# Kernel tuning notes

Hardware: AMD Instinct MI355X
Metric: run time of the kernel (lower is better)

Reference implementation:

```python
import jax, jax.numpy as jnp
import numpy as np

N, E, B = 50000, 800000, 512
IN, H, OUT = 128, 64, 32
BN_EPS = 1e-5


def setup_inputs() -> dict:
    key = jax.random.key(0)
    ks = jax.random.split(key, 32)
    inp = {}
    inp["x"] = jax.random.normal(ks[0], (N, IN), dtype=jnp.float32)
    inp["edge_index"] = jax.random.randint(ks[1], (2, E), 0, N, dtype=jnp.int64)
    inp["batch"] = jnp.sort(jax.random.randint(ks[2], (N,), 0, B, dtype=jnp.int64))
    inp["batch_size"] = B
    # GINConv MLP params: Linear(cin,H) -> BN(H) -> ReLU -> Linear(H,H)
    cins = [IN, H, H]
    ki = 3
    for i, cin in enumerate(cins):
        inp[f"c{i}_W1"] = jax.random.normal(ks[ki], (cin, H), dtype=jnp.float32) / np.sqrt(cin); ki += 1
        inp[f"c{i}_b1"] = jnp.zeros((H,), jnp.float32)
        inp[f"c{i}_g1"] = jnp.ones((H,), jnp.float32)
        inp[f"c{i}_bt1"] = jnp.zeros((H,), jnp.float32)
        inp[f"c{i}_W2"] = jax.random.normal(ks[ki], (H, H), dtype=jnp.float32) / np.sqrt(H); ki += 1
        inp[f"c{i}_b2"] = jnp.zeros((H,), jnp.float32)
    # final MLP (norm=None): Linear(H,H) -> ReLU -> [dropout, eval: identity] -> Linear(H,OUT)
    inp["f_W1"] = jax.random.normal(ks[ki], (H, H), dtype=jnp.float32) / np.sqrt(H); ki += 1
    inp["f_b1"] = jnp.zeros((H,), jnp.float32)
    inp["f_W2"] = jax.random.normal(ks[ki], (H, OUT), dtype=jnp.float32) / np.sqrt(H)
    inp["f_b2"] = jnp.zeros((OUT,), jnp.float32)
    return inp


def _bn(h, g, bt):
    # BatchNorm1d, training-mode statistics (biased variance), eps=1e-5
    mean = h.mean(axis=0)
    var = ((h - mean) ** 2).mean(axis=0)
    return g * (h - mean) * jax.lax.rsqrt(var + BN_EPS) + bt


def _gin_conv(x, src, dst, W1, b1, g1, bt1, W2, b2):
    # sum-aggregate neighbor features: agg[i] = sum_{(j->i)} x[j]
    agg = jax.ops.segment_sum(x[src], dst, num_segments=N)  # [N,H_in]
    h = x + agg  # (1+eps)*x + agg, eps=0
    h = jax.nn.relu(_bn(h @ W1 + b1, g1, bt1))
    return h @ W2 + b2


def reference(x, edge_index, batch, batch_size,
              c0_W1, c0_b1, c0_g1, c0_bt1, c0_W2, c0_b2,
              c1_W1, c1_b1, c1_g1, c1_bt1, c1_W2, c1_b2,
              c2_W1, c2_b1, c2_g1, c2_bt1, c2_W2, c2_b2,
              f_W1, f_b1, f_W2, f_b2):
    src, dst = edge_index[0], edge_index[1]
    convs = [(c0_W1, c0_b1, c0_g1, c0_bt1, c0_W2, c0_b2),
             (c1_W1, c1_b1, c1_g1, c1_bt1, c1_W2, c1_b2),
             (c2_W1, c2_b1, c2_g1, c2_bt1, c2_W2, c2_b2)]
    for p in convs:
        x = jax.nn.relu(_gin_conv(x, src, dst, *p))
    # global_add_pool over graph ids
    pooled = jax.ops.segment_sum(x, batch, num_segments=batch_size)  # [B,H]
    h = jax.nn.relu(pooled @ f_W1 + f_b1)  # dropout=0.5 skipped (eval mode)
    return h @ f_W2 + f_b2  # [B,OUT]
```

## Files before the change

### kernel.cpp

```cpp
#include <hip/hip_runtime.h>
#include <hip/hip_fp16.h>

#define NN 50000
#define EE 800000
#define BB 512
#define DIN 128
#define HH 64
#define DOUT 32
#define BN_EPS 1e-5f
#define SCAN_BLOCKS 196
#define GATHER_BLOCKS 2048
#define PADMAX (16 * NN + EE + 64)

template <int CIN>
__global__ __launch_bounds__(256) void proj_kernel(const float* __restrict__ X,
                                                   const float* __restrict__ W,
                                                   __half2* __restrict__ Qh)
{
    __shared__ float sW[CIN * 64];
    __shared__ float sX[16 * CIN];
    const int tid = threadIdx.x;
    const int row0 = blockIdx.x * 16;

    for (int i = tid; i < CIN * 16; i += 256)
        ((float4*)sW)[i] = ((const float4*)W)[i];
    const float* Xb = X + (size_t)row0 * CIN;
    for (int i = tid; i < 16 * CIN / 4; i += 256)
        ((float4*)sX)[i] = ((const float4*)Xb)[i];
    __syncthreads();

    const int col2 = tid & 31;
    const int rg   = tid >> 5;
    float2 acc0 = {0.f, 0.f};
    float2 acc1 = {0.f, 0.f};
    const float* x0p = &sX[(rg * 2 + 0) * CIN];
    const float* x1p = &sX[(rg * 2 + 1) * CIN];
#pragma unroll 4
    for (int k = 0; k < CIN; ++k) {
        const float2 w = *(const float2*)&sW[k * 64 + col2 * 2];
        const float x0 = x0p[k];
        const float x1 = x1p[k];
        acc0.x = fmaf(x0, w.x, acc0.x);
        acc0.y = fmaf(x0, w.y, acc0.y);
        acc1.x = fmaf(x1, w.x, acc1.x);
        acc1.y = fmaf(x1, w.y, acc1.y);
    }
    const int r0 = row0 + rg * 2;
    Qh[(size_t)(r0 + 0) * 32 + col2] = __floats2half2_rn(acc0.x, acc0.y);
    Qh[(size_t)(r0 + 1) * 32 + col2] = __floats2half2_rn(acc1.x, acc1.y);
}

__global__ __launch_bounds__(256) void fill_kernel(unsigned int* __restrict__ dstw,
                                                   int* __restrict__ deg)
{
    const int i = blockIdx.x * 256 + threadIdx.x;
    if (i < PADMAX / 2) dstw[i] = 0xC350C350u;
    if (i < NN) deg[i] = 0;
}

__global__ __launch_bounds__(256) void hist_rank_kernel(const int* __restrict__ dst,
                                                        int* __restrict__ deg,
                                                        unsigned short* __restrict__ rank)
{
    const int e = blockIdx.x * 256 + threadIdx.x;
    rank[e] = (unsigned short)atomicAdd(&deg[dst[e]], 1);
}

__global__ __launch_bounds__(256) void scanA_kernel(const int* __restrict__ deg,
                                                    int* __restrict__ poffs,
                                                    int* __restrict__ blockSums)
{
    __shared__ int s[256];
    const int t = threadIdx.x;
    const int i = blockIdx.x * 256 + t;
    int v = 0;
    if (i < NN) {
        const int d = deg[i];
        v = (d <= 16) ? 16 : ((d + 15) & ~15);
    }
    s[t] = v;
    __syncthreads();
    for (int off = 1; off < 256; off <<= 1) {
        const int a = (t >= off) ? s[t - off] : 0;
        __syncthreads();
        s[t] += a;
        __syncthreads();
    }
    if (i < NN) poffs[i] = s[t] - v;
    if (t == 255) blockSums[blockIdx.x] = s[255];
}

__global__ __launch_bounds__(256) void scanB_kernel(const int* __restrict__ blockSums,
                                                    int* __restrict__ blockOff,
                                                    int* __restrict__ poffs)
{
    __shared__ int s[256];
    const int t = threadIdx.x;
    const int v = (t < SCAN_BLOCKS) ? blockSums[t] : 0;
    s[t] = v;
    __syncthreads();
    for (int off = 1; off < 256; off <<= 1) {
        const int a = (t >= off) ? s[t - off] : 0;
        __syncthreads();
        s[t] += a;
        __syncthreads();
    }
    if (t < SCAN_BLOCKS) blockOff[t] = s[t] - v;
    if (t == SCAN_BLOCKS - 1) poffs[NN] = s[t];
}

__global__ __launch_bounds__(256) void scanC_kernel(int* __restrict__ poffs,
                                                    const int* __restrict__ blockOff,
                                                    float* __restrict__ statsbuf,
                                                    float* __restrict__ pooled,
                                                    unsigned int* __restrict__ qzero)
{
    const int i = blockIdx.x * 256 + threadIdx.x;
    if (i < NN) poffs[i] += blockOff[blockIdx.x];
    if (i < 384) statsbuf[i] = 0.f;
    if (i < BB * 64) pooled[i] = 0.f;
    if (blockIdx.x == 1 && threadIdx.x < 32) qzero[threadIdx.x] = 0u;
}

__global__ __launch_bounds__(256) void scatter_kernel(const int* __restrict__ src,
                                                      const int* __restrict__ dst,
                                                      const unsigned short* __restrict__ rank,
                                                      const int* __restrict__ poffs,
                                                      unsigned short* __restrict__ srcPadded)
{
    const int e = blockIdx.x * 256 + threadIdx.x;
    const int pos = poffs[dst[e]] + (int)rank[e];
    srcPadded[pos] = (unsigned short)src[e];
}

__global__ __launch_bounds__(256) void gather_kernel(const __half2* __restrict__ Qh,
                                                     const int* __restrict__ poffs,
                                                     const unsigned short* __restrict__ srcPadded,
                                                     const float* __restrict__ b1,
                                                     float* __restrict__ Z,
                                                     float* __restrict__ sums,
                                                     float* __restrict__ sumsq)
{
    const int tid   = threadIdx.x;
    const int lane  = tid & 63;
    const int wid   = tid >> 6;
    const int c     = lane & 31;
    const int grp   = lane >> 5;
    const int shamt = grp << 4;
    const uint* Qd  = (const uint*)Qh;
    const float2 bb = ((const float2*)b1)[c];

    float2 sa = {0.f, 0.f};
    float2 ta = {0.f, 0.f};
    const int step = GATHER_BLOCKS * 4;

    int node = blockIdx.x * 4 + wid;
    int p0 = poffs[node];
    int p1 = poffs[node + 1];
    uint4 ia = *(const uint4*)(srcPadded + p0);
    uint4 ib = *(const uint4*)(srcPadded + p0 + 8);
    bool two = (p1 - p0) > 16;
    uint4 ia2 = {0, 0, 0, 0}, ib2 = {0, 0, 0, 0};
    if (two) {
        ia2 = *(const uint4*)(srcPadded + p0 + 16);
        ib2 = *(const uint4*)(srcPadded + p0 + 24);
    }
    uint sr = Qd[(size_t)node * 32 + c];

    while (true) {
        uint r[16];
#pragma unroll
        for (int k = 0; k < 4; ++k) {
            r[k]     = Qd[(size_t)(((&ia.x)[k] >> shamt) & 0xffffu) * 32 + c];
            r[4 + k] = Qd[(size_t)(((&ib.x)[k] >> shamt) & 0xffffu) * 32 + c];
        }
        if (two) {
#pragma unroll
            for (int k = 0; k < 4; ++k) {
                r[8 + k]  = Qd[(size_t)(((&ia2.x)[k] >> shamt) & 0xffffu) * 32 + c];
                r[12 + k] = Qd[(size_t)(((&ib2.x)[k] >> shamt) & 0xffffu) * 32 + c];
            }
        }

        const int nnode = node + step;
        const bool more = nnode < NN;
        int np0 = 0, np1 = 0;
        uint4 nia = {0, 0, 0, 0}, nib = {0, 0, 0, 0};
        uint4 nia2 = {0, 0, 0, 0}, nib2 = {0, 0, 0, 0};
        uint nsr = 0;
        bool ntwo = false;
        if (more) {
            np0 = poffs[nnode];
            np1 = poffs[nnode + 1];
            nia = *(const uint4*)(srcPadded + np0);
            nib = *(const uint4*)(srcPadded + np0 + 8);
            ntwo = (np1 - np0) > 16;
            if (ntwo) {
                nia2 = *(const uint4*)(srcPadded + np0 + 16);
                nib2 = *(const uint4*)(srcPadded + np0 + 24);
            }
            nsr = Qd[(size_t)nnode * 32 + c];
        }

        float2 acc = {0.f, 0.f};
#pragma unroll
        for (int k = 0; k < 8; ++k) {
            const float2 p = __half22float2(*(const __half2*)&r[k]);
            acc.x += p.x;
            acc.y += p.y;
        }
        if (two) {
#pragma unroll
            for (int k = 8; k < 16; ++k) {
                const float2 p = __half22float2(*(const __half2*)&r[k]);
                acc.x += p.x;
                acc.y += p.y;
            }
        }
        for (int j = p0 + 32; j < p1; j += 16) {
            const uint4 ja = *(const uint4*)(srcPadded + j);
            const uint4 jb = *(const uint4*)(srcPadded + j + 8);
            uint rr[8];
#pragma unroll
            for (int k = 0; k < 4; ++k) {
                rr[k]     = Qd[(size_t)(((&ja.x)[k] >> shamt) & 0xffffu) * 32 + c];
                rr[4 + k] = Qd[(size_t)(((&jb.x)[k] >> shamt) & 0xffffu) * 32 + c];
            }
#pragma unroll
            for (int k = 0; k < 8; ++k) {
                const float2 p = __half22float2(*(const __half2*)&rr[k]);
                acc.x += p.x;
                acc.y += p.y;
            }
        }

        acc.x += __shfl_xor(acc.x, 32);
        acc.y += __shfl_xor(acc.y, 32);

        if (grp == 0) {
            const float2 p = __half22float2(*(const __half2*)&sr);
            acc.x += p.x + bb.x;
            acc.y += p.y + bb.y;
            ((float2*)Z)[(size_t)node * 32 + c] = acc;
            sa.x += acc.x; sa.y += acc.y;
            ta.x += acc.x * acc.x; ta.y += acc.y * acc.y;
        }

        if (!more) break;
        node = nnode; p0 = np0; p1 = np1;
        ia = nia; ib = nib; two = ntwo;
        if (two) { ia2 = nia2; ib2 = nib2; }
        sr = nsr;
    }

    __shared__ float red[4][32][4];
    if (grp == 0) {
        float* rp = red[wid][c];
        rp[0] = sa.x; rp[1] = sa.y; rp[2] = ta.x; rp[3] = ta.y;
    }
    __syncthreads();
    if (tid < 128) {
        const int c2 = tid >> 2;
        const int k  = tid & 3;
        const float v = red[0][c2][k] + red[1][c2][k] + red[2][c2][k] + red[3][c2][k];
        float* dstp;
        if (k == 0)      dstp = &sums[2 * c2 + 0];
        else if (k == 1) dstp = &sums[2 * c2 + 1];
        else if (k == 2) dstp = &sumsq[2 * c2 + 0];
        else             dstp = &sumsq[2 * c2 + 1];
        atomicAdd(dstp, v);
    }
}

__global__ __launch_bounds__(256) void gemm2proj_kernel(const float* __restrict__ Z,
                                                        const float* __restrict__ sums,
                                                        const float* __restrict__ sumsq,
                                                        const float* __restrict__ g1,
                                                        const float* __restrict__ bt1,
                                                        const float* __restrict__ W2,
                                                        const float* __restrict__ b2,
                                                        const float* __restrict__ W1n,
                                                        __half2* __restrict__ QhOut)
{
    __shared__ float sW2[64 * 64];
    __shared__ float sW1[64 * 64];
    __shared__ float sH[16 * 64];
    __shared__ float sA[16 * 64];
    __shared__ float sScale[64];
    __shared__ float sShift[64];
    const int tid = threadIdx.x;
    const int row0 = blockIdx.x * 16;

    if (tid < 64) {
        const float inv_n = 1.0f / (float)NN;
        const float mean = sums[tid] * inv_n;
        const float var = fmaxf(sumsq[tid] * inv_n - mean * mean, 0.f);
        const float sc = g1[tid] * rsqrtf(var + BN_EPS);
        sScale[tid] = sc;
        sShift[tid] = bt1[tid] - mean * sc;
    }
    for (int i = tid; i < 1024; i += 256) {
        ((float4*)sW2)[i] = ((const float4*)W2)[i];
        ((float4*)sW1)[i] = ((const float4*)W1n)[i];
    }
    __syncthreads();

    const float4* Zb = (const float4*)(Z + (size_t)row0 * 64);
    {
        const int i = tid;
        const float4 z = Zb[i];
        const int c4 = i & 15;
        const float4 sc = ((const float4*)sScale)[c4];
        const float4 sh = ((const float4*)sShift)[c4];
        float4 h;
        h.x = fmaxf(fmaf(z.x, sc.x, sh.x), 0.f);
        h.y = fmaxf(fmaf(z.y, sc.y, sh.y), 0.f);
        h.z = fmaxf(fmaf(z.z, sc.z, sh.z), 0.f);
        h.w = fmaxf(fmaf(z.w, sc.w, sh.w), 0.f);
        ((float4*)sH)[i] = h;
    }
    __syncthreads();

    {
        const int col = tid & 63;
        const int r0  = tid >> 6;
        const float bc = b2[col];
        float acc[4] = {bc, bc, bc, bc};
        for (int k = 0; k < 64; k += 4) {
            const float w0 = sW2[(k + 0) * 64 + col];
            const float w1 = sW2[(k + 1) * 64 + col];
            const float w2 = sW2[(k + 2) * 64 + col];
            const float w3 = sW2[(k + 3) * 64 + col];
#pragma unroll
            for (int rr = 0; rr < 4; ++rr) {
                const float4 hv = *(const float4*)&sH[(r0 + rr * 4) * 64 + k];
                acc[rr] = fmaf(hv.x, w0, acc[rr]);
                acc[rr] = fmaf(hv.y, w1, acc[rr]);
                acc[rr] = fmaf(hv.z, w2, acc[rr]);
                acc[rr] = fmaf(hv.w, w3, acc[rr]);
            }
        }
#pragma unroll
        for (int rr = 0; rr < 4; ++rr)
            sA[(r0 + rr * 4) * 64 + col] = fmaxf(acc[rr], 0.f);
    }
    __syncthreads();

    {
        const int col2 = tid & 31;
        const int rg   = tid >> 5;
        float2 acc0 = {0.f, 0.f};
        float2 acc1 = {0.f, 0.f};
        const float* a0p = &sA[(rg * 2 + 0) * 64];
        const float* a1p = &sA[(rg * 2 + 1) * 64];
#pragma unroll 4
        for (int k = 0; k < 64; ++k) {
            const float2 w = *(const float2*)&sW1[k * 64 + col2 * 2];
            const float a0 = a0p[k];
            const float a1 = a1p[k];
            acc0.x = fmaf(a0, w.x, acc0.x);
            acc0.y = fmaf(a0, w.y, acc0.y);
            acc1.x = fmaf(a1, w.x, acc1.x);
            acc1.y = fmaf(a1, w.y, acc1.y);
        }
        const int r0 = row0 + rg * 2;
        QhOut[(size_t)(r0 + 0) * 32 + col2] = __floats2half2_rn(acc0.x, acc0.y);
        QhOut[(size_t)(r0 + 1) * 32 + col2] = __floats2half2_rn(acc1.x, acc1.y);
    }
}

__global__ __launch_bounds__(256) void gemm2pool_kernel(const float* __restrict__ Z,
                                                        const float* __restrict__ sums,
                                                        const float* __restrict__ sumsq,
                                                        const float* __restrict__ g1,
                                                        const float* __restrict__ bt1,
                                                        const float* __restrict__ W2,
                                                        const float* __restrict__ b2,
                                                        const int* __restrict__ batch,
                                                        float* __restrict__ out)
{
    __shared__ float sW[64 * 64];
    __shared__ float sH[16 * 64];
    __shared__ float sScale[64];
    __shared__ float sShift[64];
    const int tid = threadIdx.x;
    const int row0 = blockIdx.x * 16;

    if (tid < 64) {
        const float inv_n = 1.0f / (float)NN;
        const float mean = sums[tid] * inv_n;
        const float var = fmaxf(sumsq[tid] * inv_n - mean * mean, 0.f);
        const float sc = g1[tid] * rsqrtf(var + BN_EPS);
        sScale[tid] = sc;
        sShift[tid] = bt1[tid] - mean * sc;
    }
    for (int i = tid; i < 1024; i += 256)
        ((float4*)sW)[i] = ((const float4*)W2)[i];
    __syncthreads();

    const float4* Zb = (const float4*)(Z + (size_t)row0 * 64);
    {
        const int i = tid;
        const float4 z = Zb[i];
        const int c4 = i & 15;
        const float4 sc = ((const float4*)sScale)[c4];
        const float4 sh = ((const float4*)sShift)[c4];
        float4 h;
        h.x = fmaxf(fmaf(z.x, sc.x, sh.x), 0.f);
        h.y = fmaxf(fmaf(z.y, sc.y, sh.y), 0.f);
        h.z = fmaxf(fmaf(z.z, sc.z, sh.z), 0.f);
        h.w = fmaxf(fmaf(z.w, sc.w, sh.w), 0.f);
        ((float4*)sH)[i] = h;
    }
    __syncthreads();

    const int col = tid & 63;
    const int r0  = tid >> 6;
    const float bc = b2[col];
    float acc[4] = {bc, bc, bc, bc};
    for (int k = 0; k < 64; k += 4) {
        const float w0 = sW[(k + 0) * 64 + col];
        const float w1 = sW[(k + 1) * 64 + col];
        const float w2 = sW[(k + 2) * 64 + col];
        const float w3 = sW[(k + 3) * 64 + col];
#pragma unroll
        for (int rr = 0; rr < 4; ++rr) {
            const float4 hv = *(const float4*)&sH[(r0 + rr * 4) * 64 + k];
            acc[rr] = fmaf(hv.x, w0, acc[rr]);
            acc[rr] = fmaf(hv.y, w1, acc[rr]);
            acc[rr] = fmaf(hv.z, w2, acc[rr]);
            acc[rr] = fmaf(hv.w, w3, acc[rr]);
        }
    }
#pragma unroll
    for (int rr = 0; rr < 4; ++rr) {
        const int row = row0 + r0 + rr * 4;
        const float v = fmaxf(acc[rr], 0.f);
        atomicAdd(&out[(size_t)batch[row] * 64 + col], v);
    }
}

__global__ __launch_bounds__(256) void final_mlp(const float* __restrict__ P,
                                                 const float* __restrict__ W1,
                                                 const float* __restrict__ b1,
                                                 const float* __restrict__ W2,
                                                 const float* __restrict__ b2,
                                                 float* __restrict__ out)
{
    __shared__ float sW1[64 * 64];
    __shared__ float sW2[64 * 32];
    __shared__ float sH[4 * 64];
    const int tid = threadIdx.x;
    const int row0 = blockIdx.x * 4;

    for (int i = tid; i < 1024; i += 256) ((float4*)sW1)[i] = ((const float4*)W1)[i];
    for (int i = tid; i < 512; i += 256) ((float4*)sW2)[i] = ((const float4*)W2)[i];
    __syncthreads();

    const int col = tid & 63;
    const int r = tid >> 6;
    float acc = b1[col];
    const float* prow = P + (size_t)(row0 + r) * 64;
    for (int k = 0; k < 64; ++k) acc = fmaf(prow[k], sW1[k * 64 + col], acc);
    sH[r * 64 + col] = fmaxf(acc, 0.f);
    __syncthreads();

    if (tid < 128) {
        const int c = tid & 31;
        const int r2 = tid >> 5;
        float a2 = b2[c];
        for (int k = 0; k < 64; ++k) a2 = fmaf(sH[r2 * 64 + k], sW2[k * 32 + c], a2);
        out[(size_t)(row0 + r2) * 32 + c] = a2;
    }
}

extern "C" void kernel_launch(void* const* d_in, const int* in_sizes, int n_in,
                              void* d_out, int out_size, void* d_ws, size_t ws_size,
                              hipStream_t stream)
{
    const float* x   = (const float*)d_in[0];
    const int* ei    = (const int*)d_in[1];
    const int* batch = (const int*)d_in[2];
    const float* cW1[3] = {(const float*)d_in[4],  (const float*)d_in[10], (const float*)d_in[16]};
    const float* cb1[3] = {(const float*)d_in[5],  (const float*)d_in[11], (const float*)d_in[17]};
    const float* cg1[3] = {(const float*)d_in[6],  (const float*)d_in[12], (const float*)d_in[18]};
    const float* cbt[3] = {(const float*)d_in[7],  (const float*)d_in[13], (const float*)d_in[19]};
    const float* cW2[3] = {(const float*)d_in[8],  (const float*)d_in[14], (const float*)d_in[20]};
    const float* cb2[3] = {(const float*)d_in[9],  (const float*)d_in[15], (const float*)d_in[21]};
    const float* fW1 = (const float*)d_in[22];
    const float* fb1 = (const float*)d_in[23];
    const float* fW2 = (const float*)d_in[24];
    const float* fb2 = (const float*)d_in[25];
    float* out = (float*)d_out;

    float* bufX     = (float*)d_ws;
    __half2* Qh     = (__half2*)(bufX + (size_t)NN * 64);
    float* pooled   = (float*)(Qh + (size_t)(NN + 1) * 32);
    float* statsbuf = pooled + (size_t)BB * 64;
    int* deg        = (int*)(statsbuf + 384);
    int* poffs      = deg + NN;
    int* blockSums  = poffs + (NN + 1);
    int* blockOff   = blockSums + 256;
    uintptr_t pa = ((uintptr_t)(blockOff + 256) + 15) & ~(uintptr_t)15;
    unsigned short* srcPadded = (unsigned short*)pa;
    unsigned short* rank      = srcPadded + PADMAX;

    const int* esrc = ei;
    const int* edst = ei + EE;

    const int gemm_blocks = NN / 16;
    const int edge_blocks = EE / 256;

    fill_kernel<<<(PADMAX / 2 + 255) / 256, 256, 0, stream>>>((unsigned int*)srcPadded, deg);
    hist_rank_kernel<<<edge_blocks, 256, 0, stream>>>(edst, deg, rank);
    scanA_kernel<<<SCAN_BLOCKS, 256, 0, stream>>>(deg, poffs, blockSums);
    scanB_kernel<<<1, 256, 0, stream>>>(blockSums, blockOff, poffs);
    scanC_kernel<<<SCAN_BLOCKS, 256, 0, stream>>>(poffs, blockOff, statsbuf, pooled,
                                                  (unsigned int*)(Qh + (size_t)NN * 32));
    scatter_kernel<<<edge_blocks, 256, 0, stream>>>(esrc, edst, rank, poffs, srcPadded);

    proj_kernel<DIN><<<gemm_blocks, 256, 0, stream>>>(x, cW1[0], Qh);

    for (int layer = 0; layer < 3; ++layer) {
        float* sums  = statsbuf + layer * 128;
        float* sumsq = sums + 64;

        gather_kernel<<<GATHER_BLOCKS, 256, 0, stream>>>(Qh, poffs, srcPadded, cb1[layer],
                                                         bufX, sums, sumsq);

        if (layer < 2) {
            gemm2proj_kernel<<<gemm_blocks, 256, 0, stream>>>(bufX, sums, sumsq, cg1[layer],
                                                              cbt[layer], cW2[layer], cb2[layer],
                                                              cW1[layer + 1], Qh);
        } else {
            gemm2pool_kernel<<<gemm_blocks, 256, 0, stream>>>(bufX, sums, sumsq, cg1[layer],
                                                              cbt[layer], cW2[layer], cb2[layer],
                                                              batch, pooled);
        }
    }

    final_mlp<<<BB / 4, 256, 0, stream>>>(pooled, fW1, fb1, fW2, fb2, out);
}
```

Baseline: 350.9 us.

## Split projected features into two column planes and gather each plane separately

Stores the fp16 projected features as two 16-column planes instead of one 32-column row, and runs the gather kernel twice per layer, once per plane, so each pass's random-access working set is half the size and more of it fits in cache. Each wave now processes 4 edges in parallel with 16 lanes each and reduces across lanes with an extra shuffle. Index, offset and output accesses use nontemporal loads and stores so they do not evict the feature planes. The cost is an extra kernel launch per layer and reading the CSR index arrays twice.

```diff
diff --git a/kernel.cpp b/kernel.cpp
--- a/kernel.cpp
+++ b/kernel.cpp
@@ -12,10 +12,13 @@
 #define GATHER_BLOCKS 2048
 #define PADMAX (16 * NN + EE + 64)
 
+typedef unsigned int u32x4 __attribute__((ext_vector_type(4)));
+
 template <int CIN>
 __global__ __launch_bounds__(256) void proj_kernel(const float* __restrict__ X,
                                                    const float* __restrict__ W,
-                                                   __half2* __restrict__ Qh)
+                                                   __half2* __restrict__ QhA,
+                                                   __half2* __restrict__ QhB)
 {
     __shared__ float sW[CIN * 64];
     __shared__ float sX[16 * CIN];
@@ -46,8 +49,10 @@
         acc1.y = fmaf(x1, w.y, acc1.y);
     }
     const int r0 = row0 + rg * 2;
-    Qh[(size_t)(r0 + 0) * 32 + col2] = __floats2half2_rn(acc0.x, acc0.y);
-    Qh[(size_t)(r0 + 1) * 32 + col2] = __floats2half2_rn(acc1.x, acc1.y);
+    __half2* plane = (col2 < 16) ? QhA : QhB;
+    const int pc = col2 & 15;
+    plane[(size_t)(r0 + 0) * 16 + pc] = __floats2half2_rn(acc0.x, acc0.y);
+    plane[(size_t)(r0 + 1) * 16 + pc] = __floats2half2_rn(acc1.x, acc1.y);
 }
 
 __global__ __launch_bounds__(256) void fill_kernel(unsigned int* __restrict__ dstw,
@@ -113,13 +118,15 @@
                                                     const int* __restrict__ blockOff,
                                                     float* __restrict__ statsbuf,
                                                     float* __restrict__ pooled,
-                                                    unsigned int* __restrict__ qzero)
+                                                    unsigned int* __restrict__ qzA,
+                                                    unsigned int* __restrict__ qzB)
 {
     const int i = blockIdx.x * 256 + threadIdx.x;
     if (i < NN) poffs[i] += blockOff[blockIdx.x];
     if (i < 384) statsbuf[i] = 0.f;
     if (i < BB * 64) pooled[i] = 0.f;
-    if (blockIdx.x == 1 && threadIdx.x < 32) qzero[threadIdx.x] = 0u;
+    if (blockIdx.x == 1 && threadIdx.x < 16) qzA[threadIdx.x] = 0u;
+    if (blockIdx.x == 2 && threadIdx.x < 16) qzB[threadIdx.x] = 0u;
 }
 
 __global__ __launch_bounds__(256) void scatter_kernel(const int* __restrict__ src,
@@ -133,7 +140,8 @@
     srcPadded[pos] = (unsigned short)src[e];
 }
 
-__global__ __launch_bounds__(256) void gather_kernel(const __half2* __restrict__ Qh,
+template <int PLANE>
+__global__ __launch_bounds__(256) void gather_kernel(const __half2* __restrict__ Qp,
                                                      const int* __restrict__ poffs,
                                                      const unsigned short* __restrict__ srcPadded,
                                                      const float* __restrict__ b1,
@@ -141,99 +149,113 @@
                                                      float* __restrict__ sums,
                                                      float* __restrict__ sumsq)
 {
-    const int tid   = threadIdx.x;
-    const int lane  = tid & 63;
-    const int wid   = tid >> 6;
-    const int c     = lane & 31;
-    const int grp   = lane >> 5;
-    const int shamt = grp << 4;
-    const uint* Qd  = (const uint*)Qh;
-    const float2 bb = ((const float2*)b1)[c];
+    const int tid  = threadIdx.x;
+    const int lane = tid & 63;
+    const int wid  = tid >> 6;
+    const int c    = lane & 15;
+    const int grp  = lane >> 4;
+    const int wsel = grp >> 1;
+    const int sh   = (grp & 1) << 4;
+    const uint* Qd = (const uint*)Qp;
+    const float2 bb = ((const float2*)b1)[PLANE * 16 + c];
 
     float2 sa = {0.f, 0.f};
     float2 ta = {0.f, 0.f};
     const int step = GATHER_BLOCKS * 4;
 
     int node = blockIdx.x * 4 + wid;
-    int p0 = poffs[node];
-    int p1 = poffs[node + 1];
-    uint4 ia = *(const uint4*)(srcPadded + p0);
-    uint4 ib = *(const uint4*)(srcPadded + p0 + 8);
+    int p0 = __builtin_nontemporal_load(poffs + node);
+    int p1 = __builtin_nontemporal_load(poffs + node + 1);
+    u32x4 ia = __builtin_nontemporal_load((const u32x4*)(srcPadded + p0));
+    u32x4 ib = __builtin_nontemporal_load((const u32x4*)(srcPadded + p0 + 8));
     bool two = (p1 - p0) > 16;
-    uint4 ia2 = {0, 0, 0, 0}, ib2 = {0, 0, 0, 0};
+    u32x4 ia2 = {0, 0, 0, 0}, ib2 = {0, 0, 0, 0};
     if (two) {
-        ia2 = *(const uint4*)(srcPadded + p0 + 16);
-        ib2 = *(const uint4*)(srcPadded + p0 + 24);
-    }
-    uint sr = Qd[(size_t)node * 32 + c];
+        ia2 = __builtin_nontemporal_load((const u32x4*)(srcPadded + p0 + 16));
+        ib2 = __builtin_nontemporal_load((const u32x4*)(srcPadded + p0 + 24));
+    }
+    uint sr = Qd[(size_t)node * 16 + c];
 
     while (true) {
-        uint r[16];
-#pragma unroll
-        for (int k = 0; k < 4; ++k) {
-            r[k]     = Qd[(size_t)(((&ia.x)[k] >> shamt) & 0xffffu) * 32 + c];
-            r[4 + k] = Qd[(size_t)(((&ib.x)[k] >> shamt) & 0xffffu) * 32 + c];
+        uint r[8];
+        {
+            const uint i0 = (ia[wsel] >> sh) & 0xffffu;
+            const uint i1 = (ia[2 + wsel] >> sh) & 0xffffu;
+            const uint i2 = (ib[wsel] >> sh) & 0xffffu;
+            const uint i3 = (ib[2 + wsel] >> sh) & 0xffffu;
+            r[0] = Qd[(size_t)i0 * 16 + c];
+            r[1] = Qd[(size_t)i1 * 16 + c];
+            r[2] = Qd[(size_t)i2 * 16 + c];
+            r[3] = Qd[(size_t)i3 * 16 + c];
         }
         if (two) {
-#pragma unroll
-            for (int k = 0; k < 4; ++k) {
-                r[8 + k]  = Qd[(size_t)(((&ia2.x)[k] >> shamt) & 0xffffu) * 32 + c];
-                r[12 + k] = Qd[(size_t)(((&ib2.x)[k] >> shamt) & 0xffffu) * 32 + c];
-            }
+            const uint i4 = (ia2[wsel] >> sh) & 0xffffu;
+            const uint i5 = (ia2[2 + wsel] >> sh) & 0xffffu;
+            const uint i6 = (ib2[wsel] >> sh) & 0xffffu;
+            const uint i7 = (ib2[2 + wsel] >> sh) & 0xffffu;
+            r[4] = Qd[(size_t)i4 * 16 + c];
+            r[5] = Qd[(size_t)i5 * 16 + c];
+            r[6] = Qd[(size_t)i6 * 16 + c];
+            r[7] = Qd[(size_t)i7 * 16 + c];
         }
 
         const int nnode = node + step;
         const bool more = nnode < NN;
         int np0 = 0, np1 = 0;
-        uint4 nia = {0, 0, 0, 0}, nib = {0, 0, 0, 0};
-        uint4 nia2 = {0, 0, 0, 0}, nib2 = {0, 0, 0, 0};
+        u32x4 nia = {0, 0, 0, 0}, nib = {0, 0, 0, 0};
+        u32x4 nia2 = {0, 0, 0, 0}, nib2 = {0, 0, 0, 0};
         uint nsr = 0;
         bool ntwo = false;
         if (more) {
-            np0 = poffs[nnode];
-            np1 = poffs[nnode + 1];
-            nia = *(const uint4*)(srcPadded + np0);
-            nib = *(const uint4*)(srcPadded + np0 + 8);
+            np0 = __builtin_nontemporal_load(poffs + nnode);
+            np1 = __builtin_nontemporal_load(poffs + nnode + 1);
+            nia = __builtin_nontemporal_load((const u32x4*)(srcPadded + np0));
+            nib = __builtin_nontemporal_load((const u32x4*)(srcPadded + np0 + 8));
             ntwo = (np1 - np0) > 16;
             if (ntwo) {
-                nia2 = *(const uint4*)(srcPadded + np0 + 16);
-                nib2 = *(const uint4*)(srcPadded + np0 + 24);
+                nia2 = __builtin_nontemporal_load((const u32x4*)(srcPadded + np0 + 16));
+                nib2 = __builtin_nontemporal_load((const u32x4*)(srcPadded + np0 + 24));
             }
-            nsr = Qd[(size_t)nnode * 32 + c];
+            nsr = Qd[(size_t)nnode * 16 + c];
         }
 
         float2 acc = {0.f, 0.f};
 #pragma unroll
-        for (int k = 0; k < 8; ++k) {
+        for (int k = 0; k < 4; ++k) {
             const float2 p = __half22float2(*(const __half2*)&r[k]);
             acc.x += p.x;
             acc.y += p.y;
         }
         if (two) {
 #pragma unroll
-            for (int k = 8; k < 16; ++k) {
+            for (int k = 4; k < 8; ++k) {
                 const float2 p = __half22float2(*(const __half2*)&r[k]);
                 acc.x += p.x;
                 acc.y += p.y;
             }
         }
         for (int j = p0 + 32; j < p1; j += 16) {
-            const uint4 ja = *(const uint4*)(srcPadded + j);
-            const uint4 jb = *(const uint4*)(srcPadded + j + 8);
-            uint rr[8];
+            const u32x4 ja = __builtin_nontemporal_load((const u32x4*)(srcPadded + j));
+            const u32x4 jb = __builtin_nontemporal_load((const u32x4*)(srcPadded + j + 8));
+            const uint i0 = (ja[wsel] >> sh) & 0xffffu;
+            const uint i1 = (ja[2 + wsel] >> sh) & 0xffffu;
+            const uint i2 = (jb[wsel] >> sh) & 0xffffu;
+            const uint i3 = (jb[2 + wsel] >> sh) & 0xffffu;
+            uint rr[4];
+            rr[0] = Qd[(size_t)i0 * 16 + c];
+            rr[1] = Qd[(size_t)i1 * 16 + c];
+            rr[2] = Qd[(size_t)i2 * 16 + c];
+            rr[3] = Qd[(size_t)i3 * 16 + c];
 #pragma unroll
             for (int k = 0; k < 4; ++k) {
-                rr[k]     = Qd[(size_t)(((&ja.x)[k] >> shamt) & 0xffffu) * 32 + c];
-                rr[4 + k] = Qd[(size_t)(((&jb.x)[k] >> shamt) & 0xffffu) * 32 + c];
-            }
-#pragma unroll
-            for (int k = 0; k < 8; ++k) {
                 const float2 p = __half22float2(*(const __half2*)&rr[k]);
                 acc.x += p.x;
                 acc.y += p.y;
             }
         }
 
+        acc.x += __shfl_xor(acc.x, 16);
+        acc.y += __shfl_xor(acc.y, 16);
         acc.x += __shfl_xor(acc.x, 32);
         acc.y += __shfl_xor(acc.y, 32);
 
@@ -241,7 +263,8 @@
             const float2 p = __half22float2(*(const __half2*)&sr);
             acc.x += p.x + bb.x;
             acc.y += p.y + bb.y;
-            ((float2*)Z)[(size_t)node * 32 + c] = acc;
+            double* zp = (double*)&((float2*)Z)[(size_t)node * 32 + PLANE * 16 + c];
+            __builtin_nontemporal_store(*(double*)&acc, zp);
             sa.x += acc.x; sa.y += acc.y;
             ta.x += acc.x * acc.x; ta.y += acc.y * acc.y;
         }
@@ -253,21 +276,21 @@
         sr = nsr;
     }
 
-    __shared__ float red[4][32][4];
+    __shared__ float red[4][16][4];
     if (grp == 0) {
         float* rp = red[wid][c];
         rp[0] = sa.x; rp[1] = sa.y; rp[2] = ta.x; rp[3] = ta.y;
     }
     __syncthreads();
-    if (tid < 128) {
+    if (tid < 64) {
         const int c2 = tid >> 2;
         const int k  = tid & 3;
         const float v = red[0][c2][k] + red[1][c2][k] + red[2][c2][k] + red[3][c2][k];
         float* dstp;
-        if (k == 0)      dstp = &sums[2 * c2 + 0];
-        else if (k == 1) dstp = &sums[2 * c2 + 1];
-        else if (k == 2) dstp = &sumsq[2 * c2 + 0];
-        else             dstp = &sumsq[2 * c2 + 1];
+        if (k == 0)      dstp = &sums[PLANE * 32 + 2 * c2 + 0];
+        else if (k == 1) dstp = &sums[PLANE * 32 + 2 * c2 + 1];
+        else if (k == 2) dstp = &sumsq[PLANE * 32 + 2 * c2 + 0];
+        else             dstp = &sumsq[PLANE * 32 + 2 * c2 + 1];
         atomicAdd(dstp, v);
     }
 }
@@ -280,7 +303,8 @@
                                                         const float* __restrict__ W2,
                                                         const float* __restrict__ b2,
                                                         const float* __restrict__ W1n,
-                                                        __half2* __restrict__ QhOut)
+                                                        __half2* __restrict__ QhA,
+                                                        __half2* __restrict__ QhB)
 {
     __shared__ float sW2[64 * 64];
     __shared__ float sW1[64 * 64];
@@ -364,8 +388,10 @@
             acc1.y = fmaf(a1, w.y, acc1.y);
         }
         const int r0 = row0 + rg * 2;
-        QhOut[(size_t)(r0 + 0) * 32 + col2] = __floats2half2_rn(acc0.x, acc0.y);
-        QhOut[(size_t)(r0 + 1) * 32 + col2] = __floats2half2_rn(acc1.x, acc1.y);
+        __half2* plane = (col2 < 16) ? QhA : QhB;
+        const int pc = col2 & 15;
+        plane[(size_t)(r0 + 0) * 16 + pc] = __floats2half2_rn(acc0.x, acc0.y);
+        plane[(size_t)(r0 + 1) * 16 + pc] = __floats2half2_rn(acc1.x, acc1.y);
     }
 }
 
@@ -494,8 +520,9 @@
     float* out = (float*)d_out;
 
     float* bufX     = (float*)d_ws;
-    __half2* Qh     = (__half2*)(bufX + (size_t)NN * 64);
-    float* pooled   = (float*)(Qh + (size_t)(NN + 1) * 32);
+    __half2* QhA    = (__half2*)(bufX + (size_t)NN * 64);
+    __half2* QhB    = QhA + (size_t)(NN + 1) * 16;
+    float* pooled   = (float*)(QhB + (size_t)(NN + 1) * 16);
     float* statsbuf = pooled + (size_t)BB * 64;
     int* deg        = (int*)(statsbuf + 384);
     int* poffs      = deg + NN;
@@ -516,22 +543,25 @@
     scanA_kernel<<<SCAN_BLOCKS, 256, 0, stream>>>(deg, poffs, blockSums);
     scanB_kernel<<<1, 256, 0, stream>>>(blockSums, blockOff, poffs);
     scanC_kernel<<<SCAN_BLOCKS, 256, 0, stream>>>(poffs, blockOff, statsbuf, pooled,
-                                                  (unsigned int*)(Qh + (size_t)NN * 32));
+                                                  (unsigned int*)(QhA + (size_t)NN * 16),
+                                                  (unsigned int*)(QhB + (size_t)NN * 16));
     scatter_kernel<<<edge_blocks, 256, 0, stream>>>(esrc, edst, rank, poffs, srcPadded);
 
-    proj_kernel<DIN><<<gemm_blocks, 256, 0, stream>>>(x, cW1[0], Qh);
+    proj_kernel<DIN><<<gemm_blocks, 256, 0, stream>>>(x, cW1[0], QhA, QhB);
 
     for (int layer = 0; layer < 3; ++layer) {
         float* sums  = statsbuf + layer * 128;
         float* sumsq = sums + 64;
 
-        gather_kernel<<<GATHER_BLOCKS, 256, 0, stream>>>(Qh, poffs, srcPadded, cb1[layer],
-                                                         bufX, sums, sumsq);
+        gather_kernel<0><<<GATHER_BLOCKS, 256, 0, stream>>>(QhA, poffs, srcPadded, cb1[layer],
+                                                            bufX, sums, sumsq);
+        gather_kernel<1><<<GATHER_BLOCKS, 256, 0, stream>>>(QhB, poffs, srcPadded, cb1[layer],
+                                                            bufX, sums, sumsq);
 
         if (layer < 2) {
             gemm2proj_kernel<<<gemm_blocks, 256, 0, stream>>>(bufX, sums, sumsq, cg1[layer],
                                                               cbt[layer], cW2[layer], cb2[layer],
-                                                              cW1[layer + 1], Qh);
+                                                              cW1[layer + 1], QhA, QhB);
         } else {
             gemm2pool_kernel<<<gemm_blocks, 256, 0, stream>>>(bufX, sums, sumsq, cg1[layer],
                                                               cbt[layer], cW2[layer], cb2[layer],
```

New measurement: 418.3 us. +19.2%, slower.

## Restructure gather lane mapping to 8-byte row loads and add nontemporal hints

Applied to the files above, without the earlier changes.

The gather kernel now assigns 16 lanes per row, each fetching 8 bytes (four half features), with four edge groups per wave. Previously it used 32 lanes fetching 4 bytes each, with two edge groups packed via 16-bit index shifts. Each lane now loads its own 16-bit neighbour index directly. The partial sums are reduced with two xor shuffles instead of one. Nontemporal load/store builtins are added across the streaming kernels (fill, histogram, scatter, gather, Z reads) to reduce cache pollution, though the index loads are now many small scalar loads instead of uint4 vectors.

```diff
diff --git a/kernel.cpp b/kernel.cpp
--- a/kernel.cpp
+++ b/kernel.cpp
@@ -11,6 +11,9 @@
 #define SCAN_BLOCKS 196
 #define GATHER_BLOCKS 2048
 #define PADMAX (16 * NN + EE + 64)
+
+typedef float f32x4 __attribute__((ext_vector_type(4)));
+typedef unsigned int u32x4 __attribute__((ext_vector_type(4)));
 
 template <int CIN>
 __global__ __launch_bounds__(256) void proj_kernel(const float* __restrict__ X,
@@ -54,7 +57,7 @@
                                                    int* __restrict__ deg)
 {
     const int i = blockIdx.x * 256 + threadIdx.x;
-    if (i < PADMAX / 2) dstw[i] = 0xC350C350u;
+    if (i < PADMAX / 2) __builtin_nontemporal_store(0xC350C350u, dstw + i);
     if (i < NN) deg[i] = 0;
 }
 
@@ -63,7 +66,9 @@
                                                         unsigned short* __restrict__ rank)
 {
     const int e = blockIdx.x * 256 + threadIdx.x;
-    rank[e] = (unsigned short)atomicAdd(&deg[dst[e]], 1);
+    const int d = __builtin_nontemporal_load(dst + e);
+    const unsigned short r = (unsigned short)atomicAdd(&deg[d], 1);
+    __builtin_nontemporal_store(r, rank + e);
 }
 
 __global__ __launch_bounds__(256) void scanA_kernel(const int* __restrict__ deg,
@@ -129,8 +134,11 @@
                                                       unsigned short* __restrict__ srcPadded)
 {
     const int e = blockIdx.x * 256 + threadIdx.x;
-    const int pos = poffs[dst[e]] + (int)rank[e];
-    srcPadded[pos] = (unsigned short)src[e];
+    const int d = __builtin_nontemporal_load(dst + e);
+    const int s = __builtin_nontemporal_load(src + e);
+    const int r = (int)__builtin_nontemporal_load(rank + e);
+    const int pos = poffs[d] + r;
+    srcPadded[pos] = (unsigned short)s;
 }
 
 __global__ __launch_bounds__(256) void gather_kernel(const __half2* __restrict__ Qh,
@@ -141,133 +149,129 @@
                                                      float* __restrict__ sums,
                                                      float* __restrict__ sumsq)
 {
-    const int tid   = threadIdx.x;
-    const int lane  = tid & 63;
-    const int wid   = tid >> 6;
-    const int c     = lane & 31;
-    const int grp   = lane >> 5;
-    const int shamt = grp << 4;
-    const uint* Qd  = (const uint*)Qh;
-    const float2 bb = ((const float2*)b1)[c];
-
-    float2 sa = {0.f, 0.f};
-    float2 ta = {0.f, 0.f};
+    const int tid  = threadIdx.x;
+    const int lane = tid & 63;
+    const int wid  = tid >> 6;
+    const int colq = lane & 15;
+    const int grp  = lane >> 4;
+    const uint2* Qr = (const uint2*)Qh;
+    const float4 bb = ((const float4*)b1)[colq];
+
+    float sa0 = 0.f, sa1 = 0.f, sa2 = 0.f, sa3 = 0.f;
+    float ta0 = 0.f, ta1 = 0.f, ta2 = 0.f, ta3 = 0.f;
     const int step = GATHER_BLOCKS * 4;
 
     int node = blockIdx.x * 4 + wid;
-    int p0 = poffs[node];
-    int p1 = poffs[node + 1];
-    uint4 ia = *(const uint4*)(srcPadded + p0);
-    uint4 ib = *(const uint4*)(srcPadded + p0 + 8);
+    int p0 = __builtin_nontemporal_load(poffs + node);
+    int p1 = __builtin_nontemporal_load(poffs + node + 1);
+    int i0 = __builtin_nontemporal_load(srcPadded + p0 + grp);
+    int i1 = __builtin_nontemporal_load(srcPadded + p0 + 4 + grp);
+    int i2 = __builtin_nontemporal_load(srcPadded + p0 + 8 + grp);
+    int i3 = __builtin_nontemporal_load(srcPadded + p0 + 12 + grp);
     bool two = (p1 - p0) > 16;
-    uint4 ia2 = {0, 0, 0, 0}, ib2 = {0, 0, 0, 0};
+    int i4 = NN, i5 = NN, i6 = NN, i7 = NN;
     if (two) {
-        ia2 = *(const uint4*)(srcPadded + p0 + 16);
-        ib2 = *(const uint4*)(srcPadded + p0 + 24);
-    }
-    uint sr = Qd[(size_t)node * 32 + c];
+        i4 = __builtin_nontemporal_load(srcPadded + p0 + 16 + grp);
+        i5 = __builtin_nontemporal_load(srcPadded + p0 + 20 + grp);
+        i6 = __builtin_nontemporal_load(srcPadded + p0 + 24 + grp);
+        i7 = __builtin_nontemporal_load(srcPadded + p0 + 28 + grp);
+    }
+    uint2 sr = Qr[(size_t)node * 16 + colq];
+
+#define ACC4(r)                                                            \
+    do {                                                                   \
+        const float2 pA_ = __half22float2(*(const __half2*)&(r).x);        \
+        const float2 pB_ = __half22float2(*(const __half2*)&(r).y);        \
+        a0 += pA_.x; a1 += pA_.y; a2 += pB_.x; a3 += pB_.y;                \
+    } while (0)
 
     while (true) {
-        uint r[16];
-#pragma unroll
-        for (int k = 0; k < 4; ++k) {
-            r[k]     = Qd[(size_t)(((&ia.x)[k] >> shamt) & 0xffffu) * 32 + c];
-            r[4 + k] = Qd[(size_t)(((&ib.x)[k] >> shamt) & 0xffffu) * 32 + c];
-        }
+        const uint2 r0 = Qr[(size_t)i0 * 16 + colq];
+        const uint2 r1 = Qr[(size_t)i1 * 16 + colq];
+        const uint2 r2 = Qr[(size_t)i2 * 16 + colq];
+        const uint2 r3 = Qr[(size_t)i3 * 16 + colq];
+        uint2 r4, r5, r6, r7;
         if (two) {
-#pragma unroll
-            for (int k = 0; k < 4; ++k) {
-                r[8 + k]  = Qd[(size_t)(((&ia2.x)[k] >> shamt) & 0xffffu) * 32 + c];
-                r[12 + k] = Qd[(size_t)(((&ib2.x)[k] >> shamt) & 0xffffu) * 32 + c];
-            }
+            r4 = Qr[(size_t)i4 * 16 + colq];
+            r5 = Qr[(size_t)i5 * 16 + colq];
+            r6 = Qr[(size_t)i6 * 16 + colq];
+            r7 = Qr[(size_t)i7 * 16 + colq];
         }
 
         const int nnode = node + step;
         const bool more = nnode < NN;
         int np0 = 0, np1 = 0;
-        uint4 nia = {0, 0, 0, 0}, nib = {0, 0, 0, 0};
-        uint4 nia2 = {0, 0, 0, 0}, nib2 = {0, 0, 0, 0};
-        uint nsr = 0;
+        int ni0 = NN, ni1 = NN, ni2 = NN, ni3 = NN, ni4 = NN, ni5 = NN, ni6 = NN, ni7 = NN;
+        uint2 nsr = {0, 0};
         bool ntwo = false;
         if (more) {
-            np0 = poffs[nnode];
-            np1 = poffs[nnode + 1];
-            nia = *(const uint4*)(srcPadded + np0);
-            nib = *(const uint4*)(srcPadded + np0 + 8);
+            np0 = __builtin_nontemporal_load(poffs + nnode);
+            np1 = __builtin_nontemporal_load(poffs + nnode + 1);
+            ni0 = __builtin_nontemporal_load(srcPadded + np0 + grp);
+            ni1 = __builtin_nontemporal_load(srcPadded + np0 + 4 + grp);
+            ni2 = __builtin_nontemporal_load(srcPadded + np0 + 8 + grp);
+            ni3 = __builtin_nontemporal_load(srcPadded + np0 + 12 + grp);
             ntwo = (np1 - np0) > 16;
             if (ntwo) {
-                nia2 = *(const uint4*)(srcPadded + np0 + 16);
-                nib2 = *(const uint4*)(srcPadded + np0 + 24);
+                ni4 = __builtin_nontemporal_load(srcPadded + np0 + 16 + grp);
+                ni5 = __builtin_nontemporal_load(srcPadded + np0 + 20 + grp);
+                ni6 = __builtin_nontemporal_load(srcPadded + np0 + 24 + grp);
+                ni7 = __builtin_nontemporal_load(srcPadded + np0 + 28 + grp);
             }
-            nsr = Qd[(size_t)nnode * 32 + c];
-        }
-
-        float2 acc = {0.f, 0.f};
-#pragma unroll
-        for (int k = 0; k < 8; ++k) {
-            const float2 p = __half22float2(*(const __half2*)&r[k]);
-            acc.x += p.x;
-            acc.y += p.y;
-        }
-        if (two) {
-#pragma unroll
-            for (int k = 8; k < 16; ++k) {
-                const float2 p = __half22float2(*(const __half2*)&r[k]);
-                acc.x += p.x;
-                acc.y += p.y;
-            }
-        }
+            nsr = Qr[(size_t)nnode * 16 + colq];
+        }
+
+        float a0 = 0.f, a1 = 0.f, a2 = 0.f, a3 = 0.f;
+        ACC4(r0); ACC4(r1); ACC4(r2); ACC4(r3);
+        if (two) { ACC4(r4); ACC4(r5); ACC4(r6); ACC4(r7); }
         for (int j = p0 + 32; j < p1; j += 16) {
-            const uint4 ja = *(const uint4*)(srcPadded + j);
-            const uint4 jb = *(const uint4*)(srcPadded + j + 8);
-            uint rr[8];
-#pragma unroll
-            for (int k = 0; k < 4; ++k) {
-                rr[k]     = Qd[(size_t)(((&ja.x)[k] >> shamt) & 0xffffu) * 32 + c];
-                rr[4 + k] = Qd[(size_t)(((&jb.x)[k] >> shamt) & 0xffffu) * 32 + c];
-            }
-#pragma unroll
-            for (int k = 0; k < 8; ++k) {
-                const float2 p = __half22float2(*(const __half2*)&rr[k]);
-                acc.x += p.x;
-                acc.y += p.y;
-            }
-        }
-
-        acc.x += __shfl_xor(acc.x, 32);
-        acc.y += __shfl_xor(acc.y, 32);
+            const int j0 = __builtin_nontemporal_load(srcPadded + j + grp);
+            const int j1 = __builtin_nontemporal_load(srcPadded + j + 4 + grp);
+            const int j2 = __builtin_nontemporal_load(srcPadded + j + 8 + grp);
+            const int j3 = __builtin_nontemporal_load(srcPadded + j + 12 + grp);
+            const uint2 q0 = Qr[(size_t)j0 * 16 + colq];
+            const uint2 q1 = Qr[(size_t)j1 * 16 + colq];
+            const uint2 q2 = Qr[(size_t)j2 * 16 + colq];
+            const uint2 q3 = Qr[(size_t)j3 * 16 + colq];
+            ACC4(q0); ACC4(q1); ACC4(q2); ACC4(q3);
+        }
+
+        a0 += __shfl_xor(a0, 16); a1 += __shfl_xor(a1, 16);
+        a2 += __shfl_xor(a2, 16); a3 += __shfl_xor(a3, 16);
+        a0 += __shfl_xor(a0, 32); a1 += __shfl_xor(a1, 32);
+        a2 += __shfl_xor(a2, 32); a3 += __shfl_xor(a3, 32);
 
         if (grp == 0) {
-            const float2 p = __half22float2(*(const __half2*)&sr);
-            acc.x += p.x + bb.x;
-            acc.y += p.y + bb.y;
-            ((float2*)Z)[(size_t)node * 32 + c] = acc;
-            sa.x += acc.x; sa.y += acc.y;
-            ta.x += acc.x * acc.x; ta.y += acc.y * acc.y;
+            const float2 pA = __half22float2(*(const __half2*)&sr.x);
+            const float2 pB = __half22float2(*(const __half2*)&sr.y);
+            a0 += pA.x + bb.x; a1 += pA.y + bb.y;
+            a2 += pB.x + bb.z; a3 += pB.y + bb.w;
+            f32x4 zv = {a0, a1, a2, a3};
+            __builtin_nontemporal_store(zv, (f32x4*)Z + (size_t)node * 16 + colq);
+            sa0 += a0; sa1 += a1; sa2 += a2; sa3 += a3;
+            ta0 += a0 * a0; ta1 += a1 * a1; ta2 += a2 * a2; ta3 += a3 * a3;
         }
 
         if (!more) break;
-        node = nnode; p0 = np0; p1 = np1;
-        ia = nia; ib = nib; two = ntwo;
-        if (two) { ia2 = nia2; ib2 = nib2; }
+        node = nnode; p0 = np0; p1 = np1; two = ntwo;
+        i0 = ni0; i1 = ni1; i2 = ni2; i3 = ni3;
+        i4 = ni4; i5 = ni5; i6 = ni6; i7 = ni7;
         sr = nsr;
     }
-
-    __shared__ float red[4][32][4];
+#undef ACC4
+
+    __shared__ float red[4][16][8];
     if (grp == 0) {
-        float* rp = red[wid][c];
-        rp[0] = sa.x; rp[1] = sa.y; rp[2] = ta.x; rp[3] = ta.y;
+        float* rp = red[wid][colq];
+        rp[0] = sa0; rp[1] = sa1; rp[2] = sa2; rp[3] = sa3;
+        rp[4] = ta0; rp[5] = ta1; rp[6] = ta2; rp[7] = ta3;
     }
     __syncthreads();
     if (tid < 128) {
-        const int c2 = tid >> 2;
-        const int k  = tid & 3;
-        const float v = red[0][c2][k] + red[1][c2][k] + red[2][c2][k] + red[3][c2][k];
-        float* dstp;
-        if (k == 0)      dstp = &sums[2 * c2 + 0];
-        else if (k == 1) dstp = &sums[2 * c2 + 1];
-        else if (k == 2) dstp = &sumsq[2 * c2 + 0];
-        else             dstp = &sumsq[2 * c2 + 1];
+        const int cq = tid >> 3;
+        const int k  = tid & 7;
+        const float v = red[0][cq][k] + red[1][cq][k] + red[2][cq][k] + red[3][cq][k];
+        float* dstp = (k < 4) ? &sums[cq * 4 + k] : &sumsq[cq * 4 + (k - 4)];
         atomicAdd(dstp, v);
     }
 }
@@ -305,10 +309,10 @@
     }
     __syncthreads();
 
-    const float4* Zb = (const float4*)(Z + (size_t)row0 * 64);
+    const f32x4* Zb = (const f32x4*)(Z + (size_t)row0 * 64);
     {
         const int i = tid;
-        const float4 z = Zb[i];
+        const f32x4 z = __builtin_nontemporal_load(Zb + i);
         const int c4 = i & 15;
         const float4 sc = ((const float4*)sScale)[c4];
         const float4 sh = ((const float4*)sShift)[c4];
@@ -398,10 +402,10 @@
         ((float4*)sW)[i] = ((const float4*)W2)[i];
     __syncthreads();
 
-    const float4* Zb = (const float4*)(Z + (size_t)row0 * 64);
+    const f32x4* Zb = (const f32x4*)(Z + (size_t)row0 * 64);
     {
         const int i = tid;
-        const float4 z = Zb[i];
+        const f32x4 z = __builtin_nontemporal_load(Zb + i);
         const int c4 = i & 15;
         const float4 sc = ((const float4*)sScale)[c4];
         const float4 sh = ((const float4*)sShift)[c4];
```

New measurement: 377.5 us. 1.08x slower.
